# Kernel tuning notes

Hardware: AMD Instinct MI355X
Metric: run time of the kernel (lower is better)

## Reference

```python
import jax, jax.numpy as jnp
import numpy as np

K = 7          # involution kernel size
PAD = 3        # (K-1)//2
G = 4          # groups = out_channels // group_channels
GC = 16        # group_channels
EPS = 1e-5     # BatchNorm eps


def _bn(x, g, b, m, v):
    # eval-mode BatchNorm2d over channel dim of NCHW
    scale = g / jnp.sqrt(v + EPS)
    return x * scale[:, None, None] + (b - m * scale)[:, None, None]


def _conv1x1(x, w, b=None):
    y = jnp.einsum('bchw,oc->bohw', x, w)
    if b is not None:
        y = y + b[:, None, None]
    return y


def _gelu(x):
    return jax.nn.gelu(x, approximate=False)  # torch nn.GELU default (erf)


def _involution(x, wr, gr, br, mr, vr, ws, bs):
    # kernel-generation branch: 1x1 reduce -> BN -> ReLU -> 1x1 span
    r = jax.nn.relu(_bn(_conv1x1(x, wr), gr, br, mr, vr))
    w = _conv1x1(r, ws, bs)                       # [B, G*K*K, H, W]
    B, _, H, W = w.shape
    w = w.reshape(B, G, K * K, H, W)
    # unfold x into KxK patches (channel-major then row-major kernel pos, matching nn.Unfold)
    xp = jnp.pad(x, ((0, 0), (0, 0), (PAD, PAD), (PAD, PAD)))
    patches = jnp.stack([xp[:, :, i:i + H, j:j + W]
                         for i in range(K) for j in range(K)], axis=2)  # [B, C, KK, H, W]
    patches = patches.reshape(B, G, GC, K * K, H, W)
    out = jnp.einsum('bgkhw,bgckhw->bgchw', w, patches)  # per-pixel dynamic kernel apply
    return out.reshape(B, G * GC, H, W)


def setup_inputs() -> dict:
    key = jax.random.key(0)
    ks = jax.random.split(key, 24)
    B, Cin, Cout, H, W = 4, 32, 64, 128, 128
    red = Cout // 4
    n = lambda k, s, sc: jax.random.normal(k, s, jnp.float32) * sc
    u = lambda k, s: jax.random.uniform(k, s, jnp.float32, 0.5, 1.5)
    inp = {
        'x': n(ks[0], (B, Cin, H, W), 1.0),
        'w1': n(ks[1], (Cout, Cin), 0.15),
        # involution: reduce conv + BN, span conv
        'wr': n(ks[2], (red, Cout), 0.12), 'gr': u(ks[3], (red,)), 'br': n(ks[4], (red,), 0.05),
        'mr': n(ks[5], (red,), 0.05), 'vr': u(ks[6], (red,)),
        'ws': n(ks[7], (K * K * G, red), 0.1), 'bs': n(ks[8], (K * K * G,), 0.02),
        # BN after involution
        'g1': u(ks[9], (Cout,)), 'b1': n(ks[10], (Cout,), 0.05),
        'm1': n(ks[11], (Cout,), 0.05), 'v1': u(ks[12], (Cout,)),
        # convblock2
        'w2': n(ks[13], (Cout, Cout), 0.12),
        'g2': u(ks[14], (Cout,)), 'b2': n(ks[15], (Cout,), 0.05),
        'm2': n(ks[16], (Cout,), 0.05), 'v2': u(ks[17], (Cout,)),
        # mapping (residual projection) conv has bias=True by default
        'wm': n(ks[18], (Cout, Cin), 0.15), 'bmap': n(ks[19], (Cout,), 0.02),
        'gm': u(ks[20], (Cout,)), 'betam': n(ks[21], (Cout,), 0.05),
        'mm': n(ks[22], (Cout,), 0.05), 'vm': u(ks[23], (Cout,)),
    }
    return inp


def reference(x, w1, wr, gr, br, mr, vr, ws, bs, g1, b1, m1, v1,
              w2, g2, b2, m2, v2, wm, bmap, gm, betam, mm, vm):
    x1 = _gelu(_conv1x1(x, w1))                                  # convblock
    x1 = _gelu(_bn(_involution(x1, wr, gr, br, mr, vr, ws, bs),
                   g1, b1, m1, v1))                              # involution + BN + GELU
    x1 = _bn(_conv1x1(x1, w2), g2, b2, m2, v2)                   # convblock2
    skip = _bn(_conv1x1(x, wm, bmap), gm, betam, mm, vm)         # mapping (Cin != Cout)
    return _gelu(x1 + skip)
```

## Files before the change

kernel.cpp:

```cpp
#include <hip/hip_runtime.h>
#include <hip/hip_bf16.h>
#include <math.h>

#define HW    16384
#define Bsz   4
#define CIN   32
#define COUT  64
#define RED   16
#define KKN   49
#define GG    4
#define PW    134
#define PPLANE (PW*PW)

typedef __hip_bfloat16 bf16;

__device__ __forceinline__ float gelu_f(float x) {
    return 0.5f * x * (1.0f + erff(x * 0.70710678118654752f));
}
__device__ __forceinline__ void unpack_bf2(unsigned u, float& lo, float& hi) {
    lo = __uint_as_float(u << 16);
    hi = __uint_as_float(u & 0xffff0000u);
}
__device__ __forceinline__ unsigned pack_bf2(float lo, float hi) {
    unsigned a = __float_as_uint(lo), b = __float_as_uint(hi);
    a += 0x7fff + ((a >> 16) & 1);
    b += 0x7fff + ((b >> 16) & 1);
    return (a >> 16) | (b & 0xffff0000u);
}

#define OFF_RBUF  9437184
#define OFF_X2B   13631488
#define OFF_PAR   22020096
#define PW1T 0
#define PWRT 2048
#define PW2T (2048+1024)
#define PWMT (2048+1024+4096)
#define PRSH (2048+1024+4096+2048)
#define PSHC (PRSH+16)
#define PSMV (PSHC+64)
#define PSC1 (PSMV+64)
#define PSH1 (PSC1+64)

__global__ __launch_bounds__(256) void k0_zero(uint4* __restrict__ x1pad, int n16) {
    int i = blockIdx.x * 256 + threadIdx.x;
    if (i < n16) x1pad[i] = make_uint4(0u, 0u, 0u, 0u);
}

__global__ __launch_bounds__(256) void k0_prep(
    const float* __restrict__ w1, const float* __restrict__ wr,
    const float* __restrict__ gr, const float* __restrict__ br,
    const float* __restrict__ mr, const float* __restrict__ vr,
    const float* __restrict__ g1, const float* __restrict__ b1,
    const float* __restrict__ m1, const float* __restrict__ v1,
    const float* __restrict__ w2, const float* __restrict__ g2,
    const float* __restrict__ b2, const float* __restrict__ m2,
    const float* __restrict__ v2,
    const float* __restrict__ wm, const float* __restrict__ bmap,
    const float* __restrict__ gm, const float* __restrict__ betam,
    const float* __restrict__ mm, const float* __restrict__ vm,
    float* __restrict__ par)
{
    int t = threadIdx.x;
    for (int i = t; i < 2048; i += 256) {
        int c = i >> 6, o = i & 63;
        par[PW1T + i] = w1[o * CIN + c];
    }
    for (int i = t; i < 1024; i += 256) {
        int c = i >> 4, j = i & 15;
        float sc = gr[j] * rsqrtf(vr[j] + 1e-5f);
        par[PWRT + i] = wr[j * COUT + c] * sc;
    }
    for (int i = t; i < 4096; i += 256) {
        int c = i >> 6, o = i & 63;
        float s2 = g2[o] * rsqrtf(v2[o] + 1e-5f);
        float sm = gm[o] * rsqrtf(vm[o] + 1e-5f);
        par[PW2T + i] = w2[o * COUT + c] * (s2 / sm);
    }
    for (int i = t; i < 2048; i += 256) {
        int c = i >> 6, o = i & 63;
        par[PWMT + i] = wm[o * CIN + c];
    }
    if (t < 16) {
        float sc = gr[t] * rsqrtf(vr[t] + 1e-5f);
        par[PRSH + t] = br[t] - mr[t] * sc;
    }
    if (t < 64) {
        float s2 = g2[t] * rsqrtf(v2[t] + 1e-5f);
        float sm = gm[t] * rsqrtf(vm[t] + 1e-5f);
        par[PSHC + t] = (b2[t] - m2[t] * s2) + (betam[t] + (bmap[t] - mm[t]) * sm);
        par[PSMV + t] = sm;
        float s1 = g1[t] * rsqrtf(v1[t] + 1e-5f);
        par[PSC1 + t] = s1;
        par[PSH1 + t] = b1[t] - m1[t] * s1;
    }
}

__global__ __launch_bounds__(256, 4) void k1_conv1_gelu_reduce(
    const float* __restrict__ x, const float* __restrict__ par,
    unsigned* __restrict__ x1pad, float* __restrict__ rbuf)
{
    __shared__ float g_lds[COUT][65];

    int lane  = threadIdx.x & 63;
    int chunk = __builtin_amdgcn_readfirstlane(threadIdx.x >> 6);
    int b     = blockIdx.x >> 8;
    int p     = ((blockIdx.x & 255) << 6) + lane;
    int h = p >> 7, w = p & 127;

    float acc[16];
#pragma unroll
    for (int o = 0; o < 16; ++o) acc[o] = 0.f;
#pragma unroll 8
    for (int c = 0; c < CIN; ++c) {
        float xc = x[(b * CIN + c) * HW + p];
        const float* wrow = par + PW1T + c * 64 + chunk * 16;
#pragma unroll
        for (int o = 0; o < 16; ++o) acc[o] += xc * wrow[o];
    }

    unsigned pk[8];
#pragma unroll
    for (int o = 0; o < 16; ++o) {
        acc[o] = gelu_f(acc[o]);
        g_lds[chunk * 16 + o][lane] = acc[o];
    }
#pragma unroll
    for (int d = 0; d < 8; ++d) pk[d] = pack_bf2(acc[2 * d], acc[2 * d + 1]);
    unsigned* xo = x1pad + ((size_t)((b * GG + chunk) * PW + (h + 3)) * PW + (w + 3)) * 8;
    *(uint4*)xo       = make_uint4(pk[0], pk[1], pk[2], pk[3]);
    *(uint4*)(xo + 4) = make_uint4(pk[4], pk[5], pk[6], pk[7]);

    __syncthreads();

    float ra[4] = {0.f, 0.f, 0.f, 0.f};
#pragma unroll 8
    for (int c = 0; c < COUT; ++c) {
        float gv = g_lds[c][lane];
        const float* wrow = par + PWRT + c * 16 + chunk * 4;
#pragma unroll
        for (int jj = 0; jj < 4; ++jj) ra[jj] += gv * wrow[jj];
    }
    float t[4];
#pragma unroll
    for (int jj = 0; jj < 4; ++jj)
        t[jj] = fmaxf(ra[jj] + par[PRSH + chunk * 4 + jj], 0.f);
    *(float4*)&rbuf[((size_t)b * HW + p) * 16 + chunk * 4] =
        make_float4(t[0], t[1], t[2], t[3]);
}

__global__ __launch_bounds__(256, 4) void k23_involution(
    const unsigned* __restrict__ x1pad, const float* __restrict__ rbuf,
    const float* __restrict__ wsp, const float* __restrict__ bsp,
    const float* __restrict__ par, unsigned* __restrict__ x2b)
{
    int bg = blockIdx.x >> 6;
    int g = bg & 3, b = bg >> 2;
    int p = ((blockIdx.x & 63) << 8) + threadIdx.x;
    int h = p >> 7, w0 = p & 127;

    float r[RED];
    {
        const float4* rp = (const float4*)&rbuf[((size_t)b * HW + p) * 16];
        float4 r0 = rp[0], r1 = rp[1], r2 = rp[2], r3 = rp[3];
        r[0]=r0.x; r[1]=r0.y; r[2]=r0.z; r[3]=r0.w;
        r[4]=r1.x; r[5]=r1.y; r[6]=r1.z; r[7]=r1.w;
        r[8]=r2.x; r[9]=r2.y; r[10]=r2.z; r[11]=r2.w;
        r[12]=r3.x; r[13]=r3.y; r[14]=r3.z; r[15]=r3.w;
    }

    const float* wrow = wsp + g * KKN * RED;
    const float* brow = bsp + g * KKN;
    const unsigned* base = x1pad + ((size_t)(bg * PW + h) * PW + w0) * 8;

    float acc[RED];
#pragma unroll
    for (int c = 0; c < RED; ++c) acc[c] = 0.f;

#pragma unroll 1
    for (int i = 0; i < 7; ++i) {
#pragma unroll 1
        for (int j = 0; j < 7; ++j) {
            int k = i * 7 + j;
            const float* wk_row = wrow + k * RED;
            float s = brow[k];
#pragma unroll
            for (int jj = 0; jj < RED; ++jj) s += r[jj] * wk_row[jj];
            const unsigned* tp = base + (size_t)(i * PW + j) * 8;
            uint4 A = *(const uint4*)tp;
            uint4 B = *(const uint4*)(tp + 4);
            float lo, hi;
            unpack_bf2(A.x, lo, hi); acc[0] += s*lo; acc[1] += s*hi;
            unpack_bf2(A.y, lo, hi); acc[2] += s*lo; acc[3] += s*hi;
            unpack_bf2(A.z, lo, hi); acc[4] += s*lo; acc[5] += s*hi;
            unpack_bf2(A.w, lo, hi); acc[6] += s*lo; acc[7] += s*hi;
            unpack_bf2(B.x, lo, hi); acc[8] += s*lo; acc[9] += s*hi;
            unpack_bf2(B.y, lo, hi); acc[10]+= s*lo; acc[11]+= s*hi;
            unpack_bf2(B.z, lo, hi); acc[12]+= s*lo; acc[13]+= s*hi;
            unpack_bf2(B.w, lo, hi); acc[14]+= s*lo; acc[15]+= s*hi;
        }
    }

    unsigned pk[8];
#pragma unroll
    for (int d = 0; d < 8; ++d) {
        int ch0 = g * RED + 2 * d, ch1 = ch0 + 1;
        float v0 = gelu_f(par[PSC1 + ch0] * acc[2 * d]     + par[PSH1 + ch0]);
        float v1 = gelu_f(par[PSC1 + ch1] * acc[2 * d + 1] + par[PSH1 + ch1]);
        pk[d] = pack_bf2(v0, v1);
    }
    unsigned* xo = x2b + ((size_t)bg * HW + p) * 8;
    *(uint4*)xo       = make_uint4(pk[0], pk[1], pk[2], pk[3]);
    *(uint4*)(xo + 4) = make_uint4(pk[4], pk[5], pk[6], pk[7]);
}

__global__ __launch_bounds__(256, 4) void k4_final(
    const unsigned* __restrict__ x2b, const float* __restrict__ x,
    const float* __restrict__ par, float* __restrict__ out)
{
    int lane  = threadIdx.x & 63;
    int chunk = __builtin_amdgcn_readfirstlane(threadIdx.x >> 6);
    int b     = blockIdx.x >> 8;
    int p     = ((blockIdx.x & 255) << 6) + lane;

    float acc[16];
#pragma unroll
    for (int o = 0; o < 16; ++o) acc[o] = 0.f;

#pragma unroll
    for (int gg = 0; gg < GG; ++gg) {
        const unsigned* up = x2b + ((size_t)(b * GG + gg) * HW + p) * 8;
        uint4 A = *(const uint4*)up;
        uint4 B = *(const uint4*)(up + 4);
        unsigned ud[8] = {A.x, A.y, A.z, A.w, B.x, B.y, B.z, B.w};
#pragma unroll
        for (int d = 0; d < 8; ++d) {
            float lo, hi;
            unpack_bf2(ud[d], lo, hi);
            int c0 = gg * 16 + 2 * d;
            const float* wr0 = par + PW2T + c0 * 64 + chunk * 16;
            const float* wr1 = wr0 + 64;
#pragma unroll
            for (int o = 0; o < 16; ++o) acc[o] += lo * wr0[o];
#pragma unroll
            for (int o = 0; o < 16; ++o) acc[o] += hi * wr1[o];
        }
    }
#pragma unroll 8
    for (int c = 0; c < CIN; ++c) {
        float xc = x[(b * CIN + c) * HW + p];
        const float* wrow = par + PWMT + c * 64 + chunk * 16;
#pragma unroll
        for (int o = 0; o < 16; ++o) acc[o] += xc * wrow[o];
    }
#pragma unroll
    for (int o = 0; o < 16; ++o) {
        int O = chunk * 16 + o;
        out[(size_t)(b * COUT + O) * HW + p] =
            gelu_f(par[PSMV + O] * acc[o] + par[PSHC + O]);
    }
}

extern "C" void kernel_launch(void* const* d_in, const int* in_sizes, int n_in,
                              void* d_out, int out_size, void* d_ws, size_t ws_size,
                              hipStream_t stream) {
    const float* x    = (const float*)d_in[0];
    const float* w1   = (const float*)d_in[1];
    const float* wr   = (const float*)d_in[2];
    const float* gr   = (const float*)d_in[3];
    const float* br   = (const float*)d_in[4];
    const float* mr   = (const float*)d_in[5];
    const float* vr   = (const float*)d_in[6];
    const float* wsp  = (const float*)d_in[7];
    const float* bsp  = (const float*)d_in[8];
    const float* g1   = (const float*)d_in[9];
    const float* b1   = (const float*)d_in[10];
    const float* m1   = (const float*)d_in[11];
    const float* v1   = (const float*)d_in[12];
    const float* w2   = (const float*)d_in[13];
    const float* g2   = (const float*)d_in[14];
    const float* b2   = (const float*)d_in[15];
    const float* m2   = (const float*)d_in[16];
    const float* v2   = (const float*)d_in[17];
    const float* wm   = (const float*)d_in[18];
    const float* bmap = (const float*)d_in[19];
    const float* gm   = (const float*)d_in[20];
    const float* betam= (const float*)d_in[21];
    const float* mm   = (const float*)d_in[22];
    const float* vm   = (const float*)d_in[23];

    unsigned* x1pad = (unsigned*)d_ws;
    float*    rbuf  = (float*)((char*)d_ws + OFF_RBUF);
    unsigned* x2b   = (unsigned*)((char*)d_ws + OFF_X2B);
    float*    par   = (float*)((char*)d_ws + OFF_PAR);

    int n16 = (16 * PPLANE * 32) / 16;
    k0_zero<<<(n16 + 255) / 256, 256, 0, stream>>>((uint4*)x1pad, n16);
    k0_prep<<<1, 256, 0, stream>>>(w1, wr, gr, br, mr, vr, g1, b1, m1, v1,
                                   w2, g2, b2, m2, v2, wm, bmap, gm, betam,
                                   mm, vm, par);
    k1_conv1_gelu_reduce<<<Bsz * HW / 64, 256, 0, stream>>>(x, par, x1pad, rbuf);
    k23_involution<<<Bsz * GG * HW / 256, 256, 0, stream>>>(
        x1pad, rbuf, wsp, bsp, par, x2b);
    k4_final<<<Bsz * HW / 64, 256, 0, stream>>>(x2b, x, par, (float*)d_out);
}
```

Measured before the change: 174.1 us.

## Process two pixels per thread in conv kernels and merge zero-fill into prep

The conv1+reduce and final conv kernels now compute two adjacent pixels per thread. Each weight load from the parameter buffer is reused for two FMAs, and x and out are accessed as float2. Grids are halved and launch bounds drop to 2 waves per SIMD to allow 32 accumulators. The separate zero-fill kernel is folded into the prep kernel as extra blocks, removing one launch. The costs are higher register pressure and lower occupancy, and the bf16 packing in k1 becomes more complex.

```diff
diff --git a/kernel.cpp b/kernel.cpp
--- a/kernel.cpp
+++ b/kernel.cpp
@@ -11,6 +11,7 @@
 #define GG    4
 #define PW    134
 #define PPLANE (PW*PW)
+#define N16PAD 574592
 
 typedef __hip_bfloat16 bf16;
 
@@ -41,12 +42,7 @@
 #define PSC1 (PSMV+64)
 #define PSH1 (PSC1+64)
 
-__global__ __launch_bounds__(256) void k0_zero(uint4* __restrict__ x1pad, int n16) {
-    int i = blockIdx.x * 256 + threadIdx.x;
-    if (i < n16) x1pad[i] = make_uint4(0u, 0u, 0u, 0u);
-}
-
-__global__ __launch_bounds__(256) void k0_prep(
+__global__ __launch_bounds__(256) void k0_init(
     const float* __restrict__ w1, const float* __restrict__ wr,
     const float* __restrict__ gr, const float* __restrict__ br,
     const float* __restrict__ mr, const float* __restrict__ vr,
@@ -58,8 +54,13 @@
     const float* __restrict__ wm, const float* __restrict__ bmap,
     const float* __restrict__ gm, const float* __restrict__ betam,
     const float* __restrict__ mm, const float* __restrict__ vm,
-    float* __restrict__ par)
+    float* __restrict__ par, uint4* __restrict__ x1pad)
 {
+    if (blockIdx.x != 0) {
+        int i = (blockIdx.x - 1) * 256 + threadIdx.x;
+        if (i < N16PAD) x1pad[i] = make_uint4(0u, 0u, 0u, 0u);
+        return;
+    }
     int t = threadIdx.x;
     for (int i = t; i < 2048; i += 256) {
         int c = i >> 6, o = i & 63;
@@ -95,57 +96,80 @@
     }
 }
 
-__global__ __launch_bounds__(256, 4) void k1_conv1_gelu_reduce(
+__global__ __launch_bounds__(256, 2) void k1_conv1_gelu_reduce(
     const float* __restrict__ x, const float* __restrict__ par,
     unsigned* __restrict__ x1pad, float* __restrict__ rbuf)
 {
-    __shared__ float g_lds[COUT][65];
+    __shared__ float g_lds[COUT][130];
 
     int lane  = threadIdx.x & 63;
     int chunk = __builtin_amdgcn_readfirstlane(threadIdx.x >> 6);
-    int b     = blockIdx.x >> 8;
-    int p     = ((blockIdx.x & 255) << 6) + lane;
-    int h = p >> 7, w = p & 127;
-
-    float acc[16];
-#pragma unroll
-    for (int o = 0; o < 16; ++o) acc[o] = 0.f;
-#pragma unroll 8
+    int b     = blockIdx.x >> 7;
+    int pbase = (blockIdx.x & 127) << 7;
+    int p0    = pbase + lane * 2;
+    int h = p0 >> 7, w = p0 & 127;
+
+    float acc[32];
+#pragma unroll
+    for (int i = 0; i < 32; ++i) acc[i] = 0.f;
+#pragma unroll 4
     for (int c = 0; c < CIN; ++c) {
-        float xc = x[(b * CIN + c) * HW + p];
+        float2 xc = *(const float2*)&x[(b * CIN + c) * HW + p0];
         const float* wrow = par + PW1T + c * 64 + chunk * 16;
 #pragma unroll
-        for (int o = 0; o < 16; ++o) acc[o] += xc * wrow[o];
-    }
-
-    unsigned pk[8];
+        for (int o = 0; o < 16; ++o) {
+            float wv = wrow[o];
+            acc[2 * o]     += xc.x * wv;
+            acc[2 * o + 1] += xc.y * wv;
+        }
+    }
+
+    unsigned pk[16];
 #pragma unroll
     for (int o = 0; o < 16; ++o) {
-        acc[o] = gelu_f(acc[o]);
-        g_lds[chunk * 16 + o][lane] = acc[o];
-    }
-#pragma unroll
-    for (int d = 0; d < 8; ++d) pk[d] = pack_bf2(acc[2 * d], acc[2 * d + 1]);
+        float ga = gelu_f(acc[2 * o]);
+        float gb = gelu_f(acc[2 * o + 1]);
+        g_lds[chunk * 16 + o][lane * 2]     = ga;
+        g_lds[chunk * 16 + o][lane * 2 + 1] = gb;
+        acc[2 * o] = ga; acc[2 * o + 1] = gb;
+    }
+#pragma unroll
+    for (int d = 0; d < 8; ++d) {
+        pk[d]     = pack_bf2(acc[4 * d], acc[4 * d + 2]);
+        pk[8 + d] = pack_bf2(acc[4 * d + 1], acc[4 * d + 3]);
+    }
     unsigned* xo = x1pad + ((size_t)((b * GG + chunk) * PW + (h + 3)) * PW + (w + 3)) * 8;
-    *(uint4*)xo       = make_uint4(pk[0], pk[1], pk[2], pk[3]);
-    *(uint4*)(xo + 4) = make_uint4(pk[4], pk[5], pk[6], pk[7]);
+    *(uint4*)xo        = make_uint4(pk[0], pk[1], pk[2], pk[3]);
+    *(uint4*)(xo + 4)  = make_uint4(pk[4], pk[5], pk[6], pk[7]);
+    *(uint4*)(xo + 8)  = make_uint4(pk[8], pk[9], pk[10], pk[11]);
+    *(uint4*)(xo + 12) = make_uint4(pk[12], pk[13], pk[14], pk[15]);
 
     __syncthreads();
 
-    float ra[4] = {0.f, 0.f, 0.f, 0.f};
-#pragma unroll 8
+    float ra[4] = {0.f, 0.f, 0.f, 0.f}, rb[4] = {0.f, 0.f, 0.f, 0.f};
+#pragma unroll 4
     for (int c = 0; c < COUT; ++c) {
-        float gv = g_lds[c][lane];
+        float ga = g_lds[c][lane];
+        float gb = g_lds[c][64 + lane];
         const float* wrow = par + PWRT + c * 16 + chunk * 4;
 #pragma unroll
-        for (int jj = 0; jj < 4; ++jj) ra[jj] += gv * wrow[jj];
-    }
-    float t[4];
-#pragma unroll
-    for (int jj = 0; jj < 4; ++jj)
-        t[jj] = fmaxf(ra[jj] + par[PRSH + chunk * 4 + jj], 0.f);
-    *(float4*)&rbuf[((size_t)b * HW + p) * 16 + chunk * 4] =
-        make_float4(t[0], t[1], t[2], t[3]);
+        for (int jj = 0; jj < 4; ++jj) {
+            float wv = wrow[jj];
+            ra[jj] += ga * wv;
+            rb[jj] += gb * wv;
+        }
+    }
+    float ta[4], tb[4];
+#pragma unroll
+    for (int jj = 0; jj < 4; ++jj) {
+        float sh = par[PRSH + chunk * 4 + jj];
+        ta[jj] = fmaxf(ra[jj] + sh, 0.f);
+        tb[jj] = fmaxf(rb[jj] + sh, 0.f);
+    }
+    *(float4*)&rbuf[((size_t)b * HW + pbase + lane) * 16 + chunk * 4] =
+        make_float4(ta[0], ta[1], ta[2], ta[3]);
+    *(float4*)&rbuf[((size_t)b * HW + pbase + 64 + lane) * 16 + chunk * 4] =
+        make_float4(tb[0], tb[1], tb[2], tb[3]);
 }
 
 __global__ __launch_bounds__(256, 4) void k23_involution(
@@ -213,50 +237,63 @@
     *(uint4*)(xo + 4) = make_uint4(pk[4], pk[5], pk[6], pk[7]);
 }
 
-__global__ __launch_bounds__(256, 4) void k4_final(
+__global__ __launch_bounds__(256, 2) void k4_final(
     const unsigned* __restrict__ x2b, const float* __restrict__ x,
     const float* __restrict__ par, float* __restrict__ out)
 {
     int lane  = threadIdx.x & 63;
     int chunk = __builtin_amdgcn_readfirstlane(threadIdx.x >> 6);
-    int b     = blockIdx.x >> 8;
-    int p     = ((blockIdx.x & 255) << 6) + lane;
-
-    float acc[16];
-#pragma unroll
-    for (int o = 0; o < 16; ++o) acc[o] = 0.f;
+    int b     = blockIdx.x >> 7;
+    int p0    = ((blockIdx.x & 127) << 7) + lane * 2;
+
+    float acc[32];
+#pragma unroll
+    for (int i = 0; i < 32; ++i) acc[i] = 0.f;
 
 #pragma unroll
     for (int gg = 0; gg < GG; ++gg) {
-        const unsigned* up = x2b + ((size_t)(b * GG + gg) * HW + p) * 8;
-        uint4 A = *(const uint4*)up;
-        uint4 B = *(const uint4*)(up + 4);
-        unsigned ud[8] = {A.x, A.y, A.z, A.w, B.x, B.y, B.z, B.w};
+        const unsigned* up = x2b + ((size_t)(b * GG + gg) * HW + p0) * 8;
+        uint4 A0 = *(const uint4*)up;
+        uint4 B0 = *(const uint4*)(up + 4);
+        uint4 A1 = *(const uint4*)(up + 8);
+        uint4 B1 = *(const uint4*)(up + 12);
+        unsigned u0[8] = {A0.x, A0.y, A0.z, A0.w, B0.x, B0.y, B0.z, B0.w};
+        unsigned u1[8] = {A1.x, A1.y, A1.z, A1.w, B1.x, B1.y, B1.z, B1.w};
 #pragma unroll
         for (int d = 0; d < 8; ++d) {
-            float lo, hi;
-            unpack_bf2(ud[d], lo, hi);
+            float a0, a1, b0v, b1v;
+            unpack_bf2(u0[d], a0, a1);
+            unpack_bf2(u1[d], b0v, b1v);
             int c0 = gg * 16 + 2 * d;
             const float* wr0 = par + PW2T + c0 * 64 + chunk * 16;
             const float* wr1 = wr0 + 64;
 #pragma unroll
-            for (int o = 0; o < 16; ++o) acc[o] += lo * wr0[o];
-#pragma unroll
-            for (int o = 0; o < 16; ++o) acc[o] += hi * wr1[o];
-        }
-    }
-#pragma unroll 8
+            for (int o = 0; o < 16; ++o) {
+                float w0v = wr0[o], w1v = wr1[o];
+                acc[2 * o]     += a0 * w0v + a1 * w1v;
+                acc[2 * o + 1] += b0v * w0v + b1v * w1v;
+            }
+        }
+    }
+#pragma unroll 4
     for (int c = 0; c < CIN; ++c) {
-        float xc = x[(b * CIN + c) * HW + p];
+        float2 xc = *(const float2*)&x[(b * CIN + c) * HW + p0];
         const float* wrow = par + PWMT + c * 64 + chunk * 16;
 #pragma unroll
-        for (int o = 0; o < 16; ++o) acc[o] += xc * wrow[o];
+        for (int o = 0; o < 16; ++o) {
+            float wv = wrow[o];
+            acc[2 * o]     += xc.x * wv;
+            acc[2 * o + 1] += xc.y * wv;
+        }
     }
 #pragma unroll
     for (int o = 0; o < 16; ++o) {
         int O = chunk * 16 + o;
-        out[(size_t)(b * COUT + O) * HW + p] =
-            gelu_f(par[PSMV + O] * acc[o] + par[PSHC + O]);
+        float sm = par[PSMV + O], sh = par[PSHC + O];
+        float2 v;
+        v.x = gelu_f(sm * acc[2 * o]     + sh);
+        v.y = gelu_f(sm * acc[2 * o + 1] + sh);
+        *(float2*)&out[(size_t)(b * COUT + O) * HW + p0] = v;
     }
 }
 
@@ -293,13 +330,12 @@
     unsigned* x2b   = (unsigned*)((char*)d_ws + OFF_X2B);
     float*    par   = (float*)((char*)d_ws + OFF_PAR);
 
-    int n16 = (16 * PPLANE * 32) / 16;
-    k0_zero<<<(n16 + 255) / 256, 256, 0, stream>>>((uint4*)x1pad, n16);
-    k0_prep<<<1, 256, 0, stream>>>(w1, wr, gr, br, mr, vr, g1, b1, m1, v1,
-                                   w2, g2, b2, m2, v2, wm, bmap, gm, betam,
-                                   mm, vm, par);
-    k1_conv1_gelu_reduce<<<Bsz * HW / 64, 256, 0, stream>>>(x, par, x1pad, rbuf);
+    int nzb = (N16PAD + 255) / 256;
+    k0_init<<<nzb + 1, 256, 0, stream>>>(w1, wr, gr, br, mr, vr, g1, b1, m1, v1,
+                                         w2, g2, b2, m2, v2, wm, bmap, gm, betam,
+                                         mm, vm, par, (uint4*)x1pad);
+    k1_conv1_gelu_reduce<<<Bsz * HW / 128, 256, 0, stream>>>(x, par, x1pad, rbuf);
     k23_involution<<<Bsz * GG * HW / 256, 256, 0, stream>>>(
         x1pad, rbuf, wsp, bsp, par, x2b);
-    k4_final<<<Bsz * HW / 64, 256, 0, stream>>>(x2b, x, par, (float*)d_out);
-}
+    k4_final<<<Bsz * HW / 128, 256, 0, stream>>>(x2b, x, par, (float*)d_out);
+}
```

New measurement: 213.7 us. 22.7% more time.

## Use bf16 MFMA for final conv2+mapping GEMM, merge zero and prep kernels

Applied to the files above, without the earlier changes.

Replaces the scalar FMA final kernel with a bf16 MFMA 16x16x32 GEMM over the concatenated [x2 | x] channels (K=96), using the folded w2/wm weights stored as bf16. k1 now writes a bf16 pixel-major copy of x for the MFMA A-operand, and the zeroing kernel is merged into the param-prep kernel to save a launch. The cost is extra bf16 rounding of x and of the weights, plus an extra write of x in bf16 from k1.

```diff
diff --git a/kernel.cpp b/kernel.cpp
--- a/kernel.cpp
+++ b/kernel.cpp
@@ -11,8 +11,11 @@
 #define GG    4
 #define PW    134
 #define PPLANE (PW*PW)
+#define N16PAD 574592
 
 typedef __hip_bfloat16 bf16;
+typedef __attribute__((ext_vector_type(8))) short bf16x8;
+typedef __attribute__((ext_vector_type(4))) float f32x4;
 
 __device__ __forceinline__ float gelu_f(float x) {
     return 0.5f * x * (1.0f + erff(x * 0.70710678118654752f));
@@ -27,26 +30,26 @@
     b += 0x7fff + ((b >> 16) & 1);
     return (a >> 16) | (b & 0xffff0000u);
 }
+__device__ __forceinline__ unsigned short bf16r(float v) {
+    unsigned a = __float_as_uint(v);
+    a += 0x7fff + ((a >> 16) & 1);
+    return (unsigned short)(a >> 16);
+}
 
 #define OFF_RBUF  9437184
 #define OFF_X2B   13631488
 #define OFF_PAR   22020096
+#define OFF_XBF   22085632
 #define PW1T 0
 #define PWRT 2048
-#define PW2T (2048+1024)
-#define PWMT (2048+1024+4096)
-#define PRSH (2048+1024+4096+2048)
+#define PRSH 3072
 #define PSHC (PRSH+16)
 #define PSMV (PSHC+64)
 #define PSC1 (PSMV+64)
 #define PSH1 (PSC1+64)
-
-__global__ __launch_bounds__(256) void k0_zero(uint4* __restrict__ x1pad, int n16) {
-    int i = blockIdx.x * 256 + threadIdx.x;
-    if (i < n16) x1pad[i] = make_uint4(0u, 0u, 0u, 0u);
-}
-
-__global__ __launch_bounds__(256) void k0_prep(
+#define PCAT_F 12288
+
+__global__ __launch_bounds__(256) void k0_init(
     const float* __restrict__ w1, const float* __restrict__ wr,
     const float* __restrict__ gr, const float* __restrict__ br,
     const float* __restrict__ mr, const float* __restrict__ vr,
@@ -58,8 +61,13 @@
     const float* __restrict__ wm, const float* __restrict__ bmap,
     const float* __restrict__ gm, const float* __restrict__ betam,
     const float* __restrict__ mm, const float* __restrict__ vm,
-    float* __restrict__ par)
+    float* __restrict__ par, uint4* __restrict__ x1pad)
 {
+    if (blockIdx.x != 0) {
+        int i = (blockIdx.x - 1) * 256 + threadIdx.x;
+        if (i < N16PAD) x1pad[i] = make_uint4(0u, 0u, 0u, 0u);
+        return;
+    }
     int t = threadIdx.x;
     for (int i = t; i < 2048; i += 256) {
         int c = i >> 6, o = i & 63;
@@ -70,15 +78,18 @@
         float sc = gr[j] * rsqrtf(vr[j] + 1e-5f);
         par[PWRT + i] = wr[j * COUT + c] * sc;
     }
-    for (int i = t; i < 4096; i += 256) {
-        int c = i >> 6, o = i & 63;
-        float s2 = g2[o] * rsqrtf(v2[o] + 1e-5f);
-        float sm = gm[o] * rsqrtf(vm[o] + 1e-5f);
-        par[PW2T + i] = w2[o * COUT + c] * (s2 / sm);
-    }
-    for (int i = t; i < 2048; i += 256) {
-        int c = i >> 6, o = i & 63;
-        par[PWMT + i] = wm[o * CIN + c];
+    unsigned short* wcat = (unsigned short*)(par + PCAT_F);
+    for (int i = t; i < 64 * 96; i += 256) {
+        int o = i / 96, c = i - o * 96;
+        float v;
+        if (c < 64) {
+            float s2 = g2[o] * rsqrtf(v2[o] + 1e-5f);
+            float sm = gm[o] * rsqrtf(vm[o] + 1e-5f);
+            v = w2[o * COUT + c] * (s2 / sm);
+        } else {
+            v = wm[o * CIN + (c - 64)];
+        }
+        wcat[i] = bf16r(v);
     }
     if (t < 16) {
         float sc = gr[t] * rsqrtf(vr[t] + 1e-5f);
@@ -97,7 +108,8 @@
 
 __global__ __launch_bounds__(256, 4) void k1_conv1_gelu_reduce(
     const float* __restrict__ x, const float* __restrict__ par,
-    unsigned* __restrict__ x1pad, float* __restrict__ rbuf)
+    unsigned* __restrict__ x1pad, float* __restrict__ rbuf,
+    unsigned short* __restrict__ xbf)
 {
     __shared__ float g_lds[COUT][65];
 
@@ -107,12 +119,27 @@
     int p     = ((blockIdx.x & 255) << 6) + lane;
     int h = p >> 7, w = p & 127;
 
+    float xv[CIN];
+#pragma unroll
+    for (int c = 0; c < CIN; ++c) xv[c] = x[(b * CIN + c) * HW + p];
+
+    if (chunk == 0) {
+        unsigned pkx[16];
+#pragma unroll
+        for (int d = 0; d < 16; ++d) pkx[d] = pack_bf2(xv[2 * d], xv[2 * d + 1]);
+        unsigned* xo2 = (unsigned*)&xbf[((size_t)(b * HW + p)) * 32];
+        *(uint4*)xo2        = make_uint4(pkx[0], pkx[1], pkx[2], pkx[3]);
+        *(uint4*)(xo2 + 4)  = make_uint4(pkx[4], pkx[5], pkx[6], pkx[7]);
+        *(uint4*)(xo2 + 8)  = make_uint4(pkx[8], pkx[9], pkx[10], pkx[11]);
+        *(uint4*)(xo2 + 12) = make_uint4(pkx[12], pkx[13], pkx[14], pkx[15]);
+    }
+
     float acc[16];
 #pragma unroll
     for (int o = 0; o < 16; ++o) acc[o] = 0.f;
 #pragma unroll 8
     for (int c = 0; c < CIN; ++c) {
-        float xc = x[(b * CIN + c) * HW + p];
+        float xc = xv[c];
         const float* wrow = par + PW1T + c * 64 + chunk * 16;
 #pragma unroll
         for (int o = 0; o < 16; ++o) acc[o] += xc * wrow[o];
@@ -213,50 +240,53 @@
     *(uint4*)(xo + 4) = make_uint4(pk[4], pk[5], pk[6], pk[7]);
 }
 
-__global__ __launch_bounds__(256, 4) void k4_final(
-    const unsigned* __restrict__ x2b, const float* __restrict__ x,
+__global__ __launch_bounds__(256, 4) void k4_mfma(
+    const unsigned short* __restrict__ x2s, const unsigned short* __restrict__ xbf,
     const float* __restrict__ par, float* __restrict__ out)
 {
-    int lane  = threadIdx.x & 63;
-    int chunk = __builtin_amdgcn_readfirstlane(threadIdx.x >> 6);
-    int b     = blockIdx.x >> 8;
-    int p     = ((blockIdx.x & 255) << 6) + lane;
-
-    float acc[16];
-#pragma unroll
-    for (int o = 0; o < 16; ++o) acc[o] = 0.f;
-
-#pragma unroll
-    for (int gg = 0; gg < GG; ++gg) {
-        const unsigned* up = x2b + ((size_t)(b * GG + gg) * HW + p) * 8;
-        uint4 A = *(const uint4*)up;
-        uint4 B = *(const uint4*)(up + 4);
-        unsigned ud[8] = {A.x, A.y, A.z, A.w, B.x, B.y, B.z, B.w};
-#pragma unroll
-        for (int d = 0; d < 8; ++d) {
-            float lo, hi;
-            unpack_bf2(ud[d], lo, hi);
-            int c0 = gg * 16 + 2 * d;
-            const float* wr0 = par + PW2T + c0 * 64 + chunk * 16;
-            const float* wr1 = wr0 + 64;
-#pragma unroll
-            for (int o = 0; o < 16; ++o) acc[o] += lo * wr0[o];
-#pragma unroll
-            for (int o = 0; o < 16; ++o) acc[o] += hi * wr1[o];
-        }
-    }
-#pragma unroll 8
-    for (int c = 0; c < CIN; ++c) {
-        float xc = x[(b * CIN + c) * HW + p];
-        const float* wrow = par + PWMT + c * 64 + chunk * 16;
-#pragma unroll
-        for (int o = 0; o < 16; ++o) acc[o] += xc * wrow[o];
-    }
-#pragma unroll
-    for (int o = 0; o < 16; ++o) {
-        int O = chunk * 16 + o;
-        out[(size_t)(b * COUT + O) * HW + p] =
-            gelu_f(par[PSMV + O] * acc[o] + par[PSHC + O]);
+    int lane = threadIdx.x & 63;
+    int wave = threadIdx.x >> 6;
+    int m15  = lane & 15;
+    int quad = lane >> 4;
+    int b    = blockIdx.x >> 8;
+    int px0  = (((blockIdx.x & 255) << 2) + wave) << 4;
+
+    const unsigned short* wcat = (const unsigned short*)(par + PCAT_F);
+
+    bf16x8 Bf[3][4];
+#pragma unroll
+    for (int kt = 0; kt < 3; ++kt)
+#pragma unroll
+        for (int nt = 0; nt < 4; ++nt)
+            Bf[kt][nt] = *(const bf16x8*)&wcat[(nt * 16 + m15) * 96 + kt * 32 + quad * 8];
+
+    int px = px0 + m15;
+    bf16x8 Af[3];
+    {
+        int g0 = quad >> 1, co = (quad & 1) * 8;
+        Af[0] = *(const bf16x8*)&x2s[((size_t)((b * 4 + g0) * HW + px)) * 16 + co];
+        Af[1] = *(const bf16x8*)&x2s[((size_t)((b * 4 + 2 + g0) * HW + px)) * 16 + co];
+        Af[2] = *(const bf16x8*)&xbf[((size_t)(b * HW + px)) * 32 + quad * 8];
+    }
+
+    f32x4 acc[4];
+#pragma unroll
+    for (int nt = 0; nt < 4; ++nt) acc[nt] = (f32x4){0.f, 0.f, 0.f, 0.f};
+#pragma unroll
+    for (int kt = 0; kt < 3; ++kt)
+#pragma unroll
+        for (int nt = 0; nt < 4; ++nt)
+            acc[nt] = __builtin_amdgcn_mfma_f32_16x16x32_bf16(
+                Af[kt], Bf[kt][nt], acc[nt], 0, 0, 0);
+
+#pragma unroll
+    for (int nt = 0; nt < 4; ++nt) {
+        int o = nt * 16 + m15;
+        float smv = par[PSMV + o], sh = par[PSHC + o];
+        float* op = out + (size_t)(b * COUT + o) * HW + px0 + quad * 4;
+#pragma unroll
+        for (int reg = 0; reg < 4; ++reg)
+            op[reg] = gelu_f(smv * acc[nt][reg] + sh);
     }
 }
 
@@ -288,18 +318,19 @@
     const float* mm   = (const float*)d_in[22];
     const float* vm   = (const float*)d_in[23];
 
-    unsigned* x1pad = (unsigned*)d_ws;
-    float*    rbuf  = (float*)((char*)d_ws + OFF_RBUF);
-    unsigned* x2b   = (unsigned*)((char*)d_ws + OFF_X2B);
-    float*    par   = (float*)((char*)d_ws + OFF_PAR);
-
-    int n16 = (16 * PPLANE * 32) / 16;
-    k0_zero<<<(n16 + 255) / 256, 256, 0, stream>>>((uint4*)x1pad, n16);
-    k0_prep<<<1, 256, 0, stream>>>(w1, wr, gr, br, mr, vr, g1, b1, m1, v1,
-                                   w2, g2, b2, m2, v2, wm, bmap, gm, betam,
-                                   mm, vm, par);
-    k1_conv1_gelu_reduce<<<Bsz * HW / 64, 256, 0, stream>>>(x, par, x1pad, rbuf);
+    unsigned*       x1pad = (unsigned*)d_ws;
+    float*          rbuf  = (float*)((char*)d_ws + OFF_RBUF);
+    unsigned*       x2b   = (unsigned*)((char*)d_ws + OFF_X2B);
+    float*          par   = (float*)((char*)d_ws + OFF_PAR);
+    unsigned short* xbf   = (unsigned short*)((char*)d_ws + OFF_XBF);
+
+    int nzb = (N16PAD + 255) / 256;
+    k0_init<<<nzb + 1, 256, 0, stream>>>(w1, wr, gr, br, mr, vr, g1, b1, m1, v1,
+                                         w2, g2, b2, m2, v2, wm, bmap, gm, betam,
+                                         mm, vm, par, (uint4*)x1pad);
+    k1_conv1_gelu_reduce<<<Bsz * HW / 64, 256, 0, stream>>>(x, par, x1pad, rbuf, xbf);
     k23_involution<<<Bsz * GG * HW / 256, 256, 0, stream>>>(
         x1pad, rbuf, wsp, bsp, par, x2b);
-    k4_final<<<Bsz * HW / 64, 256, 0, stream>>>(x2b, x, par, (float*)d_out);
-}
+    k4_mfma<<<Bsz * HW / 64, 256, 0, stream>>>(
+        (const unsigned short*)x2b, xbf, par, (float*)d_out);
+}
```

After: 173.2 us. No clear change (-0.5%).
